# Kernel optimization log

Hardware: AMD Instinct MI355X
Metric: run time of the kernel (lower is better)

## Reference

```python
import jax, jax.numpy as jnp
import numpy as np

B, S, D = 16, 512, 2048
NUM_HEADS, NUM_GROUPS = 16, 4
HEAD_DIM = D // NUM_HEADS  # 128
MAX_SEQ_LEN, SHARED_SLOTS = 512, 32
EPS = 1e-6


def _rope_tables(seq_positions):
    # inv_freq over half the head dim, as in the module
    inv_freq = 1.0 / (10000.0 ** (jnp.arange(0, HEAD_DIM, 2, dtype=jnp.float32) / HEAD_DIM))
    freqs = jnp.outer(seq_positions.astype(jnp.float32), inv_freq)  # [S, HEAD_DIM//2]
    return jnp.cos(freqs), jnp.sin(freqs)


def _apply_rope(x, cos, sin):
    # x: [b, s, h, head_dim]; cos/sin: [s, 1, head_dim//2] (broadcast over heads)
    x1, x2 = jnp.split(x, 2, axis=-1)
    real = x1 * cos - x2 * sin
    imag = x1 * sin + x2 * cos
    return jnp.concatenate([real, imag], axis=-1).astype(x.dtype)


def _rmsnorm(x, scale):
    # flax RMSNorm with dtype=float32: compute in fp32
    x = x.astype(jnp.float32)
    ms = jnp.mean(jnp.square(x), axis=-1, keepdims=True)
    return x * jax.lax.rsqrt(ms + EPS) * scale


def setup_inputs() -> dict:
    key = jax.random.key(0)
    ks = jax.random.split(key, 10)
    w = 0.02
    return {
        "x": jax.random.normal(ks[0], (B, S, D), dtype=jnp.float32),
        "wq": jax.random.normal(ks[1], (D, D), dtype=jnp.float32) * w,
        "bq": jnp.zeros((D,), dtype=jnp.float32),
        "wk": jax.random.normal(ks[2], (D, NUM_GROUPS * HEAD_DIM), dtype=jnp.float32) * w,
        "bk": jnp.zeros((NUM_GROUPS * HEAD_DIM,), dtype=jnp.float32),
        "wv": jax.random.normal(ks[3], (D, NUM_GROUPS * HEAD_DIM), dtype=jnp.float32) * w,
        "bv": jnp.zeros((NUM_GROUPS * HEAD_DIM,), dtype=jnp.float32),
        "wo": jax.random.normal(ks[4], (D, D), dtype=jnp.float32) * w,
        "bo": jnp.zeros((D,), dtype=jnp.float32),
        "q_norm_scale": jnp.ones((HEAD_DIM,), dtype=jnp.float32),
        "k_norm_scale": jnp.ones((HEAD_DIM,), dtype=jnp.float32),
    }


def reference(x, wq, bq, wk, bk, wv, bv, wo, bo, q_norm_scale, k_norm_scale):
    b, s, d = x.shape
    rep = NUM_HEADS // NUM_GROUPS
    head_scale = HEAD_DIM ** (-0.5)  # applied once explicitly by the module

    # nnx.Linear(dtype=float16): projections computed in fp16
    xh = x.astype(jnp.float16)
    q = (xh @ wq.astype(jnp.float16) + bq.astype(jnp.float16)).reshape(b, s, NUM_HEADS, HEAD_DIM)
    k = (xh @ wk.astype(jnp.float16) + bk.astype(jnp.float16)).reshape(b, s, NUM_GROUPS, HEAD_DIM)
    v = (xh @ wv.astype(jnp.float16) + bv.astype(jnp.float16)).reshape(b, s, NUM_GROUPS, HEAD_DIM)

    # QK RMSNorm (fp32)
    q = _rmsnorm(q, q_norm_scale)
    k = _rmsnorm(k, k_norm_scale)

    # RoPE (default positions 0..s-1)
    pos = jnp.arange(s)
    cos, sin = _rope_tables(pos)
    cos = cos[:, None, :]
    sin = sin[:, None, :]
    q = _apply_rope(q, cos, sin) * head_scale
    k = _apply_rope(k, cos, sin)

    q = q.astype(jnp.float16)
    k = k.astype(jnp.float16)
    v = v.astype(jnp.float16)

    # GQA without materializing repeated k/v: [b, s, groups, rep, head_dim]
    qg = q.reshape(b, s, NUM_GROUPS, rep, HEAD_DIM)
    # dot_product_attention applies its own 1/sqrt(head_dim) (double-scale, faithful)
    logits = jnp.einsum('btgrh,bsgh->bgrts', qg, k,
                        preferred_element_type=jnp.float32) * head_scale

    causal = pos[:, None] >= pos[None, :]  # [s, s]
    logits = jnp.where(causal[None, None, None, :, :], logits, jnp.finfo(jnp.float32).min)
    probs = jax.nn.softmax(logits, axis=-1).astype(jnp.float16)

    out = jnp.einsum('bgrts,bsgh->btgrh', probs, v)  # [b, s, groups, rep, head_dim]
    out = out.reshape(b, s, d)
    return out @ wo.astype(jnp.float16) + bo.astype(jnp.float16)
```

## Files before the change

kernel.cpp:

```cpp
#include <hip/hip_runtime.h>

#define NB 16
#define NS 512
#define ND 2048
#define NH 16
#define NG 4
#define NHD 128
#define NM (NB * NS)
#define NKD (NG * NHD)
#define NKV 1024
#define HEAD_SCALE 0.08838834764831845f

typedef _Float16 h8 __attribute__((ext_vector_type(8)));
typedef float fx4 __attribute__((ext_vector_type(4)));

__device__ __forceinline__ void gload16(const void* g, void* l) {
  __builtin_amdgcn_global_load_lds(
      (__attribute__((address_space(1))) void*)(unsigned long long)g,
      (__attribute__((address_space(3))) void*)(unsigned long long)l,
      16, 0, 0);
}


__global__ void cvt_x_kernel(const float* __restrict__ in, _Float16* __restrict__ out, int n8) {
  int i = blockIdx.x * 256 + threadIdx.x;
  if (i >= n8) return;
  const fx4* p = (const fx4*)in;
  fx4 a = p[2 * i], b = p[2 * i + 1];
  h8 h;
  h[0] = (_Float16)a[0]; h[1] = (_Float16)a[1]; h[2] = (_Float16)a[2]; h[3] = (_Float16)a[3];
  h[4] = (_Float16)b[0]; h[5] = (_Float16)b[1]; h[6] = (_Float16)b[2]; h[7] = (_Float16)b[3];
  ((h8*)out)[i] = h;
}

__global__ void wtrans_kernel(const float* __restrict__ w, _Float16* __restrict__ wt, int K, int N) {
  __shared__ float t[64][65];
  int n0 = blockIdx.x * 64, k0 = blockIdx.y * 64;
#pragma unroll
  for (int it = 0; it < 16; ++it) {
    int idx = it * 256 + threadIdx.x;
    int r = idx >> 6, c = idx & 63;
    t[r][c] = w[(size_t)(k0 + r) * N + n0 + c];
  }
  __syncthreads();
#pragma unroll
  for (int it = 0; it < 16; ++it) {
    int idx = it * 256 + threadIdx.x;
    int r = idx >> 6, c = idx & 63;
    wt[(size_t)(n0 + r) * K + k0 + c] = (_Float16)t[c][r];
  }
}

__global__ void vtrans_kernel(const _Float16* __restrict__ kv, _Float16* __restrict__ vt) {
  __shared__ _Float16 t[64][72];
  int st = blockIdx.x, dt = blockIdx.y, bg = blockIdx.z;
  int b = bg >> 2, g = bg & 3;
  const _Float16* src = kv + ((size_t)(b * NS + st * 64)) * NKV + NKD + g * NHD + dt * 64;
#pragma unroll
  for (int it = 0; it < 2; ++it) {
    int idx = it * 256 + threadIdx.x;
    int r = idx >> 3, c = (idx & 7) * 8;
    *(h8*)&t[r][c] = *(const h8*)(src + (size_t)r * NKV + c);
  }
  __syncthreads();
  _Float16* dst = vt + ((size_t)bg * NHD + dt * 64) * NS + st * 64;
#pragma unroll
  for (int it = 0; it < 2; ++it) {
    int idx = it * 256 + threadIdx.x;
    int r = idx >> 3, c = (idx & 7) * 8;
    h8 o;
#pragma unroll
    for (int e = 0; e < 8; ++e) o[e] = t[c + e][r];
    *(h8*)(dst + (size_t)r * NS + c) = o;
  }
}

__global__ void rope_tables_kernel(float* __restrict__ cosT, float* __restrict__ sinT) {
  int i = blockIdx.x * 256 + threadIdx.x;
  int s = i >> 6, f = i & 63;
  float inv = exp2f(-(float)f * (13.287712379549449f / 64.0f));
  float a = (float)s * inv;
  cosT[i] = cosf(a);
  sinT[i] = sinf(a);
}

__global__ void norm_rope_kernel(_Float16* __restrict__ X, const float* __restrict__ scale,
                                 const float* __restrict__ cosT, const float* __restrict__ sinT,
                                 int hshift, int rowStride, float outScale) {
  int wid = threadIdx.x >> 6, lane = threadIdx.x & 63;
  int task = blockIdx.x * 4 + wid;
  int row = task >> hshift;
  int head = task & ((1 << hshift) - 1);
  _Float16* p = X + (size_t)row * rowStride + head * NHD;
  float x1 = (float)p[lane], x2 = (float)p[lane + 64];
  float ss = x1 * x1 + x2 * x2;
#pragma unroll
  for (int m = 1; m < 64; m <<= 1) ss += __shfl_xor(ss, m, 64);
  float rn = rsqrtf(ss * (1.0f / 128.0f) + 1e-6f);
  int s = row & (NS - 1);
  float c = cosT[s * 64 + lane], sn = sinT[s * 64 + lane];
  float n1 = x1 * rn * scale[lane], n2 = x2 * rn * scale[64 + lane];
  p[lane] = (_Float16)((n1 * c - n2 * sn) * outScale);
  p[lane + 64] = (_Float16)((n1 * sn + n2 * c) * outScale);
}

__device__ __forceinline__ void st_out(float* p, float v) { *p = v; }
__device__ __forceinline__ void st_out(_Float16* p, float v) { *p = (_Float16)v; }


template <typename OT>
__global__ __launch_bounds__(256, 3) void gemm_bt_kernel(
    const _Float16* __restrict__ A, const _Float16* __restrict__ Bt,
    const float* __restrict__ bias, OT* __restrict__ C, int N, int K) {
  __shared__ alignas(16) _Float16 As[128 * 64];
  __shared__ alignas(16) _Float16 Bs[128 * 64];
  const int tid = threadIdx.x;
  const int lane = tid & 63, wid = tid >> 6;
  const int wr = wid >> 1, wc = wid & 1;
  const int la = lane & 15, lb = (lane >> 4) * 8;
  const int bm = blockIdx.y * 128, bn = blockIdx.x * 128;

  fx4 acc[4][4] = {};

  for (int kt = 0; kt < K; kt += 64) {
    const _Float16* Ag = A + (size_t)bm * K + kt;
    const _Float16* Bg = Bt + (size_t)bn * K + kt;
#pragma unroll
    for (int it = 0; it < 4; ++it) {
      int cb = it * 256 + wid * 64;
      int ca = cb + lane;
      int r = ca >> 3, cc = ca & 7;
      gload16(Ag + (size_t)r * K + cc * 8, &As[cb * 8]);
      gload16(Bg + (size_t)r * K + cc * 8, &Bs[cb * 8]);
    }
    __syncthreads();
#pragma unroll
    for (int kk = 0; kk < 2; ++kk) {
      h8 af[4], bf[4];
#pragma unroll
      for (int m = 0; m < 4; ++m)
        af[m] = *(const h8*)&As[(wr * 64 + m * 16 + la) * 64 + kk * 32 + lb];
#pragma unroll
      for (int n = 0; n < 4; ++n)
        bf[n] = *(const h8*)&Bs[(wc * 64 + n * 16 + la) * 64 + kk * 32 + lb];
#pragma unroll
      for (int m = 0; m < 4; ++m)
#pragma unroll
        for (int n = 0; n < 4; ++n)
          acc[m][n] = __builtin_amdgcn_mfma_f32_16x16x32_f16(af[m], bf[n], acc[m][n], 0, 0, 0);
    }
    __syncthreads();
  }
#pragma unroll
  for (int m = 0; m < 4; ++m) {
    int row0 = bm + wr * 64 + m * 16 + (lane >> 4) * 4;
#pragma unroll
    for (int n = 0; n < 4; ++n) {
      int col = bn + wc * 64 + n * 16 + la;
      float bvv = bias[col];
#pragma unroll
      for (int r = 0; r < 4; ++r)
        st_out(&C[(size_t)(row0 + r) * N + col], acc[m][n][r] + bvv);
    }
  }
}


template <typename OT>
__global__ __launch_bounds__(512, 2) void gemm256_kernel(
    const _Float16* __restrict__ A, const _Float16* __restrict__ Bt,
    const float* __restrict__ bias, OT* __restrict__ C, int N, int K) {
  __shared__ alignas(16) _Float16 As[2][256 * 64];
  __shared__ alignas(16) _Float16 Bs[2][256 * 64];
  const int tid = threadIdx.x;
  const int lane = tid & 63, w = tid >> 6;
  const int wr = w >> 2, wc = w & 3;
  const int la = lane & 15, lq = lane >> 4;
  const int lin = (blockIdx.x & 7) * 32 + (blockIdx.x >> 3);
  const int nbx = N >> 8;
  const int by = lin / nbx, bx = lin % nbx;
  const int bm = by * 256, bn = bx * 256;
  const int NT = K >> 6;

  fx4 acc[8][4] = {};

  auto stage = [&](int buf, int kt) {
    const _Float16* Ag = A + (size_t)bm * K + kt * 64;
    const _Float16* Bg = Bt + (size_t)bn * K + kt * 64;
#pragma unroll
    for (int it = 0; it < 4; ++it) {
      int cb = it * 512 + w * 64;
      int s = cb + lane;
      int r = s >> 3, c = s & 7;
      int srcoff = r * K + ((c ^ (r & 7)) << 3);
      gload16(Ag + srcoff, &As[buf][cb * 8]);
      gload16(Bg + srcoff, &Bs[buf][cb * 8]);
    }
  };

  stage(0, 0);
  for (int kt = 0; kt < NT; ++kt) {
    const int cur = kt & 1;
    if (kt + 1 < NT) {
      stage(cur ^ 1, kt + 1);
      asm volatile("s_waitcnt vmcnt(8)" ::: "memory");
    } else {
      asm volatile("s_waitcnt vmcnt(0)" ::: "memory");
    }
    __builtin_amdgcn_s_barrier();
    __builtin_amdgcn_sched_barrier(0);
#pragma unroll
    for (int q = 0; q < 4; ++q) {
      h8 af[2][2], bf[4][2];
#pragma unroll
      for (int mi = 0; mi < 2; ++mi)
#pragma unroll
        for (int kk = 0; kk < 2; ++kk) {
          int row = wr * 128 + (q * 2 + mi) * 16 + la;
          int c = kk * 4 + lq;
          af[mi][kk] = *(const h8*)&As[cur][row * 64 + ((c ^ (row & 7)) << 3)];
        }
#pragma unroll
      for (int ni = 0; ni < 4; ++ni)
#pragma unroll
        for (int kk = 0; kk < 2; ++kk) {
          int row = wc * 64 + ni * 16 + la;
          int c = kk * 4 + lq;
          bf[ni][kk] = *(const h8*)&Bs[cur][row * 64 + ((c ^ (row & 7)) << 3)];
        }
      asm volatile("s_waitcnt lgkmcnt(0)" ::: "memory");
      __builtin_amdgcn_sched_barrier(0);
      __builtin_amdgcn_s_setprio(1);
#pragma unroll
      for (int mi = 0; mi < 2; ++mi)
#pragma unroll
        for (int ni = 0; ni < 4; ++ni)
#pragma unroll
          for (int kk = 0; kk < 2; ++kk)
            acc[q * 2 + mi][ni] = __builtin_amdgcn_mfma_f32_16x16x32_f16(
                af[mi][kk], bf[ni][kk], acc[q * 2 + mi][ni], 0, 0, 0);
      __builtin_amdgcn_s_setprio(0);
      __builtin_amdgcn_sched_barrier(0);
      __builtin_amdgcn_s_barrier();
    }
  }
#pragma unroll
  for (int mi = 0; mi < 8; ++mi) {
    int row0 = bm + wr * 128 + mi * 16 + lq * 4;
#pragma unroll
    for (int ni = 0; ni < 4; ++ni) {
      int col = bn + wc * 64 + ni * 16 + la;
      float bvv = bias[col];
#pragma unroll
      for (int r = 0; r < 4; ++r)
        st_out(&C[(size_t)(row0 + r) * N + col], acc[mi][ni][r] + bvv);
    }
  }
}


__global__ __launch_bounds__(512, 4) void attn_kernel(
    const _Float16* __restrict__ Q, const _Float16* __restrict__ KV,
    const _Float16* __restrict__ Vt, _Float16* __restrict__ ctx) {
  __shared__ alignas(16) _Float16 Ks[2][64 * 128];
  __shared__ alignas(16) _Float16 Vs[2][128 * 64];
  __shared__ alignas(16) _Float16 Ps[8][16 * 64];

  const int bid = blockIdx.x;
  const int logical = (bid & 7) * 64 + (bid >> 3);
  const int b = logical >> 5;
  const int g = (logical >> 3) & 3;
  const int jp = logical & 7;
  const int j1 = jp, j2 = 15 - jp;

  const int tid = threadIdx.x;
  const int lane = tid & 63, w = tid >> 6;
  const int la = lane & 15, lq = lane >> 4;
  const int h = g * 4 + (w & 3);
  const int rh = w >> 2;

  const _Float16* Vg = Vt + (size_t)(b * NG + g) * NHD * NS;

  auto stage = [&](int buf, int kt) {
    const _Float16* Kg = KV + ((size_t)(b * NS + kt * 64)) * NKV + g * NHD;
#pragma unroll
    for (int it = 0; it < 2; ++it) {
      int cb = it * 512 + w * 64;
      int s = cb + lane;
      int rr = s >> 4, c = s & 15;
      gload16(Kg + (size_t)rr * NKV + ((c ^ (rr & 7)) * 8), &Ks[buf][cb * 8]);
    }
#pragma unroll
    for (int it = 0; it < 2; ++it) {
      int cb = it * 512 + w * 64;
      int s = cb + lane;
      int rr = s >> 3, c = s & 7;
      gload16(Vg + (size_t)rr * NS + kt * 64 + ((c ^ (rr & 7)) * 8), &Vs[buf][cb * 8]);
    }
  };

  const int nt1 = ((j1 * 32 + 31) >> 6) + 1;
  const int nt2 = ((j2 * 32 + 31) >> 6) + 1;
  const int ntotal = nt1 + nt2;

  h8 qf[4];
  fx4 oacc[8];
  float mrun[4], lrun[4];

  stage(0, 0);
  int cur = 0;
  for (int t = 0; t < ntotal; ++t) {
    const bool inA = t < nt1;
    const int j = inA ? j1 : j2;
    const int kt = inA ? t : t - nt1;
    const int ntj = inA ? nt1 : nt2;
    __syncthreads();
    if (t + 1 < ntotal) {
      int nkt = (t + 1 < nt1) ? (t + 1) : (t + 1 - nt1);
      stage(cur ^ 1, nkt);
    }
    if (kt == 0) {
      const _Float16* Qg = Q + ((size_t)(b * NS + j * 32 + rh * 16 + la)) * ND + h * NHD + lq * 8;
#pragma unroll
      for (int kc = 0; kc < 4; ++kc) qf[kc] = *(const h8*)(Qg + kc * 32);
#pragma unroll
      for (int f = 0; f < 8; ++f) oacc[f] = fx4{0.f, 0.f, 0.f, 0.f};
#pragma unroll
      for (int r = 0; r < 4; ++r) { mrun[r] = -1e30f; lrun[r] = 0.f; }
    }

    fx4 sc[4] = {};
    __builtin_amdgcn_s_setprio(1);
#pragma unroll
    for (int n = 0; n < 4; ++n) {
      int row = n * 16 + la;
#pragma unroll
      for (int kc = 0; kc < 4; ++kc) {
        h8 bk = *(const h8*)&Ks[cur][row * 128 + (((kc * 4 + lq) ^ (la & 7)) * 8)];
        sc[n] = __builtin_amdgcn_mfma_f32_16x16x32_f16(qf[kc], bk, sc[n], 0, 0, 0);
      }
    }
    __builtin_amdgcn_s_setprio(0);

    const int qrow0 = j * 32 + rh * 16 + lq * 4;
    const bool maskT = (kt == ntj - 1);
    float pv[4][4];
    float rm[4] = {-1e30f, -1e30f, -1e30f, -1e30f};
#pragma unroll
    for (int n = 0; n < 4; ++n) {
      int kv = kt * 64 + n * 16 + la;
#pragma unroll
      for (int r = 0; r < 4; ++r) {
        float sv = sc[n][r] * HEAD_SCALE;
        sv = (maskT && kv > qrow0 + r) ? -1e30f : sv;
        pv[n][r] = sv;
        rm[r] = fmaxf(rm[r], sv);
      }
    }
#pragma unroll
    for (int r = 0; r < 4; ++r) {
#pragma unroll
      for (int m = 1; m < 16; m <<= 1) rm[r] = fmaxf(rm[r], __shfl_xor(rm[r], m, 64));
      float mn = fmaxf(mrun[r], rm[r]);
      float corr = __expf(mrun[r] - mn);
      mrun[r] = mn;
      lrun[r] *= corr;
#pragma unroll
      for (int f = 0; f < 8; ++f) oacc[f][r] *= corr;
    }
    float rs[4] = {0.f, 0.f, 0.f, 0.f};
#pragma unroll
    for (int n = 0; n < 4; ++n)
#pragma unroll
      for (int r = 0; r < 4; ++r) {
        float e = __expf(pv[n][r] - mrun[r]);
        pv[n][r] = e;
        rs[r] += e;
      }
#pragma unroll
    for (int r = 0; r < 4; ++r) {
#pragma unroll
      for (int m = 1; m < 16; m <<= 1) rs[r] += __shfl_xor(rs[r], m, 64);
      lrun[r] += rs[r];
    }

#pragma unroll
    for (int n = 0; n < 4; ++n)
#pragma unroll
      for (int r = 0; r < 4; ++r) {
        int row = lq * 4 + r;
        int chsw = (n * 2 + (la >> 3)) ^ (row & 7);
        Ps[w][row * 64 + chsw * 8 + (la & 7)] = (_Float16)pv[n][r];
      }
    asm volatile("s_waitcnt lgkmcnt(0)" ::: "memory");
    __builtin_amdgcn_sched_barrier(0);
    h8 pf[2];
#pragma unroll
    for (int ks = 0; ks < 2; ++ks)
      pf[ks] = *(const h8*)&Ps[w][la * 64 + (((ks * 4 + lq) ^ (la & 7)) * 8)];

    __builtin_amdgcn_s_setprio(1);
#pragma unroll
    for (int f = 0; f < 8; ++f) {
      int row = f * 16 + la;
#pragma unroll
      for (int ks = 0; ks < 2; ++ks) {
        h8 bv = *(const h8*)&Vs[cur][row * 64 + (((ks * 4 + lq) ^ (la & 7)) * 8)];
        oacc[f] = __builtin_amdgcn_mfma_f32_16x16x32_f16(pf[ks], bv, oacc[f], 0, 0, 0);
      }
    }
    __builtin_amdgcn_s_setprio(0);

    if (maskT) {
      _Float16* Cg = ctx + ((size_t)(b * NS + qrow0)) * ND + h * NHD + la;
      float inv_l[4];
#pragma unroll
      for (int r = 0; r < 4; ++r) inv_l[r] = 1.0f / lrun[r];
#pragma unroll
      for (int f = 0; f < 8; ++f)
#pragma unroll
        for (int r = 0; r < 4; ++r)
          Cg[(size_t)r * ND + f * 16] = (_Float16)(oacc[f][r] * inv_l[r]);
    }
    cur ^= 1;
  }
}


extern "C" void kernel_launch(void* const* d_in, const int* in_sizes, int n_in,
                              void* d_out, int out_size, void* d_ws, size_t ws_size,
                              hipStream_t stream) {
  (void)in_sizes; (void)n_in; (void)out_size; (void)ws_size;
  const float* x = (const float*)d_in[0];
  const float* wq = (const float*)d_in[1];
  const float* bq = (const float*)d_in[2];
  const float* wk = (const float*)d_in[3];
  const float* bk = (const float*)d_in[4];
  const float* wv = (const float*)d_in[5];
  const float* bv = (const float*)d_in[6];
  const float* wo = (const float*)d_in[7];
  const float* bo = (const float*)d_in[8];
  const float* qns = (const float*)d_in[9];
  const float* kns = (const float*)d_in[10];

  char* ws = (char*)d_ws;
  size_t off = 0;
  _Float16* xh = (_Float16*)(ws + off); off += (size_t)NM * ND * 2;
  _Float16* wqt = (_Float16*)(ws + off); off += (size_t)ND * ND * 2;
  _Float16* wkvt = (_Float16*)(ws + off); off += (size_t)NKV * ND * 2;
  _Float16* wot = (_Float16*)(ws + off); off += (size_t)ND * ND * 2;
  _Float16* Qb = (_Float16*)(ws + off); off += (size_t)NM * ND * 2;
  _Float16* KVbuf = (_Float16*)(ws + off); off += (size_t)NM * NKV * 2;
  float* cosT = (float*)(ws + off); off += (size_t)NS * 64 * 4;
  float* sinT = (float*)(ws + off); off += (size_t)NS * 64 * 4;
  float* bkv = (float*)(ws + off); off += (size_t)NKV * 4;
  _Float16* ctx = xh;
  _Float16* Vtg = wqt;

  cvt_x_kernel<<<NM * ND / 8 / 256, 256, 0, stream>>>(x, xh, NM * ND / 8);
  wtrans_kernel<<<dim3(ND / 64, ND / 64), 256, 0, stream>>>(wq, wqt, ND, ND);
  wtrans_kernel<<<dim3(NKD / 64, ND / 64), 256, 0, stream>>>(wk, wkvt, ND, NKD);
  wtrans_kernel<<<dim3(NKD / 64, ND / 64), 256, 0, stream>>>(wv, wkvt + (size_t)NKD * ND, ND, NKD);
  wtrans_kernel<<<dim3(ND / 64, ND / 64), 256, 0, stream>>>(wo, wot, ND, ND);
  rope_tables_kernel<<<NS * 64 / 256, 256, 0, stream>>>(cosT, sinT);
  hipMemcpyAsync(bkv, bk, NKD * sizeof(float), hipMemcpyDeviceToDevice, stream);
  hipMemcpyAsync(bkv + NKD, bv, NKD * sizeof(float), hipMemcpyDeviceToDevice, stream);

  gemm256_kernel<_Float16><<<dim3(256), dim3(512), 0, stream>>>(xh, wqt, bq, Qb, ND, ND);
  gemm_bt_kernel<_Float16><<<dim3(NKV / 128, NM / 128), 256, 0, stream>>>(xh, wkvt, bkv, KVbuf, NKV, ND);

  norm_rope_kernel<<<NM * NH / 4, 256, 0, stream>>>(Qb, qns, cosT, sinT, 4, ND, HEAD_SCALE);
  norm_rope_kernel<<<NM * NG / 4, 256, 0, stream>>>(KVbuf, kns, cosT, sinT, 2, NKV, 1.0f);

  vtrans_kernel<<<dim3(NS / 64, NHD / 64, NB * NG), 256, 0, stream>>>(KVbuf, Vtg);

  attn_kernel<<<dim3(512), dim3(512), 0, stream>>>(Qb, KVbuf, Vtg, ctx);

  gemm256_kernel<float><<<dim3(256), dim3(512), 0, stream>>>(ctx, wot, bo, (float*)d_out, ND, ND);
}
```

Baseline: 321.9 us.

## Split gemm256 K-tile into half-slabs and interleave prefetch with MFMA phases

Restructures the 256x256 GEMM main loop so each 64-wide K tile is stored as two 32-wide LDS half-slabs with a new XOR swizzle. Global-to-LDS prefetch of the next tile is spread across four compute phases instead of issued all at once, with partial vmcnt waits between phases. B fragments are reused across two A-row groups per phase. The aim is finer overlap of global loads with MFMA work and fewer LDS fragment reads. In exchange it adds more barriers per tile and a more intricate wait/barrier ordering that could stall or race if the counts are wrong.

```diff
diff --git a/kernel.cpp b/kernel.cpp
--- a/kernel.cpp
+++ b/kernel.cpp
@@ -170,8 +170,8 @@
 __global__ __launch_bounds__(512, 2) void gemm256_kernel(
     const _Float16* __restrict__ A, const _Float16* __restrict__ Bt,
     const float* __restrict__ bias, OT* __restrict__ C, int N, int K) {
-  __shared__ alignas(16) _Float16 As[2][256 * 64];
-  __shared__ alignas(16) _Float16 Bs[2][256 * 64];
+  __shared__ alignas(16) _Float16 As[2][2][256 * 32];
+  __shared__ alignas(16) _Float16 Bs[2][2][256 * 32];
   const int tid = threadIdx.x;
   const int lane = tid & 63, w = tid >> 6;
   const int wr = w >> 2, wc = w & 3;
@@ -184,61 +184,79 @@
 
   fx4 acc[8][4] = {};
 
-  auto stage = [&](int buf, int kt) {
-    const _Float16* Ag = A + (size_t)bm * K + kt * 64;
-    const _Float16* Bg = Bt + (size_t)bn * K + kt * 64;
-#pragma unroll
-    for (int it = 0; it < 4; ++it) {
-      int cb = it * 512 + w * 64;
-      int s = cb + lane;
-      int r = s >> 3, c = s & 7;
-      int srcoff = r * K + ((c ^ (r & 7)) << 3);
-      gload16(Ag + srcoff, &As[buf][cb * 8]);
-      gload16(Bg + srcoff, &Bs[buf][cb * 8]);
-    }
-  };
-
-  stage(0, 0);
+  {
+    const _Float16* Ag = A + (size_t)bm * K;
+    const _Float16* Bg = Bt + (size_t)bn * K;
+#pragma unroll
+    for (int sh = 0; sh < 2; ++sh) {
+#pragma unroll
+      for (int i = 0; i < 2; ++i) {
+        int cb = i * 512 + w * 64;
+        int s = cb + lane;
+        int r = s >> 2, c = s & 3;
+        gload16(Ag + (size_t)r * K + sh * 32 + ((c ^ ((r >> 1) & 3)) << 3), &As[0][sh][cb * 8]);
+      }
+#pragma unroll
+      for (int i = 0; i < 2; ++i) {
+        int cb = i * 512 + w * 64;
+        int s = cb + lane;
+        int r = s >> 2, c = s & 3;
+        gload16(Bg + (size_t)r * K + sh * 32 + ((c ^ ((r >> 1) & 3)) << 3), &Bs[0][sh][cb * 8]);
+      }
+    }
+  }
+  asm volatile("s_waitcnt vmcnt(4)" ::: "memory");
+  __builtin_amdgcn_s_barrier();
+
   for (int kt = 0; kt < NT; ++kt) {
     const int cur = kt & 1;
-    if (kt + 1 < NT) {
-      stage(cur ^ 1, kt + 1);
-      asm volatile("s_waitcnt vmcnt(8)" ::: "memory");
-    } else {
-      asm volatile("s_waitcnt vmcnt(0)" ::: "memory");
-    }
-    __builtin_amdgcn_s_barrier();
-    __builtin_amdgcn_sched_barrier(0);
-#pragma unroll
-    for (int q = 0; q < 4; ++q) {
-      h8 af[2][2], bf[4][2];
-#pragma unroll
-      for (int mi = 0; mi < 2; ++mi)
-#pragma unroll
-        for (int kk = 0; kk < 2; ++kk) {
-          int row = wr * 128 + (q * 2 + mi) * 16 + la;
-          int c = kk * 4 + lq;
-          af[mi][kk] = *(const h8*)&As[cur][row * 64 + ((c ^ (row & 7)) << 3)];
+    const int nxt = cur ^ 1;
+    const bool more = (kt + 1 < NT);
+    const _Float16* Ag = A + (size_t)bm * K + (kt + 1) * 64;
+    const _Float16* Bg = Bt + (size_t)bn * K + (kt + 1) * 64;
+    h8 bf[4];
+#pragma unroll
+    for (int ph = 0; ph < 4; ++ph) {
+      const int kh = ph >> 1, g = ph & 1;
+      h8 af[4];
+#pragma unroll
+      for (int mi = 0; mi < 4; ++mi) {
+        int row = wr * 128 + (g * 4 + mi) * 16 + la;
+        af[mi] = *(const h8*)&As[cur][kh][row * 32 + ((lq ^ ((row >> 1) & 3)) << 3)];
+      }
+      if (g == 0) {
+#pragma unroll
+        for (int ni = 0; ni < 4; ++ni) {
+          int row = wc * 64 + ni * 16 + la;
+          bf[ni] = *(const h8*)&Bs[cur][kh][row * 32 + ((lq ^ ((row >> 1) & 3)) << 3)];
         }
-#pragma unroll
-      for (int ni = 0; ni < 4; ++ni)
-#pragma unroll
-        for (int kk = 0; kk < 2; ++kk) {
-          int row = wc * 64 + ni * 16 + la;
-          int c = kk * 4 + lq;
-          bf[ni][kk] = *(const h8*)&Bs[cur][row * 64 + ((c ^ (row & 7)) << 3)];
+      }
+      if (more) {
+        const int sh = ph >> 1;
+        const _Float16* Sg = (ph & 1) ? Bg : Ag;
+        _Float16* Ld = (ph & 1) ? &Bs[nxt][sh][0] : &As[nxt][sh][0];
+#pragma unroll
+        for (int i = 0; i < 2; ++i) {
+          int cb = i * 512 + w * 64;
+          int s = cb + lane;
+          int r = s >> 2, c = s & 3;
+          gload16(Sg + (size_t)r * K + sh * 32 + ((c ^ ((r >> 1) & 3)) << 3), Ld + cb * 8);
         }
+      }
+      if (ph == 1 || ph == 3) {
+        if (more) asm volatile("s_waitcnt vmcnt(4)" ::: "memory");
+        else      asm volatile("s_waitcnt vmcnt(0)" ::: "memory");
+      }
+      __builtin_amdgcn_s_barrier();
       asm volatile("s_waitcnt lgkmcnt(0)" ::: "memory");
       __builtin_amdgcn_sched_barrier(0);
       __builtin_amdgcn_s_setprio(1);
 #pragma unroll
-      for (int mi = 0; mi < 2; ++mi)
+      for (int mi = 0; mi < 4; ++mi)
 #pragma unroll
         for (int ni = 0; ni < 4; ++ni)
-#pragma unroll
-          for (int kk = 0; kk < 2; ++kk)
-            acc[q * 2 + mi][ni] = __builtin_amdgcn_mfma_f32_16x16x32_f16(
-                af[mi][kk], bf[ni][kk], acc[q * 2 + mi][ni], 0, 0, 0);
+          acc[g * 4 + mi][ni] = __builtin_amdgcn_mfma_f32_16x16x32_f16(
+              af[mi], bf[ni], acc[g * 4 + mi][ni], 0, 0, 0);
       __builtin_amdgcn_s_setprio(0);
       __builtin_amdgcn_sched_barrier(0);
       __builtin_amdgcn_s_barrier();
```

Result: faster. 308.5 us (-4.2%).
